# Performance work log

Hardware: AMD Instinct MI355X
Metric: run time of the kernel (lower is better)

Reference implementation:

```python
import jax, jax.numpy as jnp
import numpy as np

N, C, H, W = 64, 512, 16, 16
MEM_DIM, NUM_CLS = 2000, 10


def setup_inputs() -> dict:
    key = jax.random.key(0)
    k1, k2, k3 = jax.random.split(key, 3)
    z = jax.random.normal(k1, (N, C, H, W), dtype=jnp.float32)
    cls = jax.random.randint(k2, (N,), 0, NUM_CLS, dtype=jnp.int32)
    # nn.init.normal_(memory, 0.0, 0.02)
    memory = 0.02 * jax.random.normal(k3, (1, C, MEM_DIM, NUM_CLS), dtype=jnp.float32)
    return {"z": z, "cls": cls, "memory": memory}


def reference(z, cls, memory):
    n, c, h, w_ = z.shape
    hw = h * w_
    # memory[0,:,:,cls] -> (C, M, N) -> per-sample class memory (N, C, M)
    mem_cls = jnp.transpose(memory[0][:, :, cls], (2, 0, 1))  # (N, C, M)
    zf = z.reshape(n, c, hw)  # (N, C, HW)
    # similarity = -||z - m||^2 = 2 z.m - ||z||^2 - ||m||^2
    zm = jnp.einsum('ncp,ncm->npm', zf, mem_cls)          # (N, HW, M)
    z2 = jnp.sum(zf * zf, axis=1)[:, :, None]             # (N, HW, 1)
    m2 = jnp.sum(mem_cls * mem_cls, axis=1)[:, None, :]   # (N, 1, M)
    sim = 2.0 * zm - z2 - m2                               # (N, HW, M)
    log_w = jax.nn.log_softmax(sim, axis=2)
    w = jax.nn.softmax(sim, axis=2)
    w_hat = w  # topk == -1 in forward path
    # z_hat = bmm(mem_cls (N,C,M), w_hat^T (N,M,HW)) -> (N,C,HW)
    z_hat = jnp.einsum('ncm,npm->ncp', mem_cls, w_hat).reshape(n, c, h, w_)
    return (z_hat, w_hat, w, log_w)
```

## Files before the change

### kernel.cpp

```cpp
#include <hip/hip_runtime.h>
#include <hip/hip_bf16.h>
#include <math.h>

#define N_   64
#define C_   512
#define HW_  256
#define M_   2000
#define KCLS 10
#define MP_  2048

typedef __attribute__((ext_vector_type(8))) short bf16x8;
typedef __attribute__((ext_vector_type(4))) float f32x4;

__device__ __forceinline__ short f2bf(float x) {
    __hip_bfloat16 b = __float2bfloat16(x);
    return *reinterpret_cast<short*>(&b);
}
__device__ __forceinline__ float bf2f(short s) {
    __hip_bfloat16 b = *reinterpret_cast<__hip_bfloat16*>(&s);
    return __bfloat162float(b);
}

#define GATHER_LDS (KCLS * 32 * 66 * 2)
#define PART_LDS   (KCLS * 8 * 32 * 4)

__global__ __launch_bounds__(256) void prep_kernel(const float* __restrict__ mem,
                                                   const float* __restrict__ z,
                                                   const int* __restrict__ cls,
                                                   short* __restrict__ mcm,
                                                   short* __restrict__ mmc,
                                                   short* __restrict__ zTb,
                                                   float* __restrict__ m2,
                                                   int* __restrict__ perm) {
    __shared__ __align__(16) char smem[GATHER_LDS + PART_LDS];
    const int t = threadIdx.x;
    const int bid = blockIdx.x;

    if (bid < 512) {
        short (*tile)[32][66] = reinterpret_cast<short(*)[32][66]>(smem);
        float (*part)[8][32]  = reinterpret_cast<float(*)[8][32]>(smem + GATHER_LDS);
        const int m0 = (bid & 63) * 32;
        const int c0 = (bid >> 6) * 64;
        const int mm = t & 31;
        const int m = m0 + mm;
        const int cbase = t >> 5;
        float msum[KCLS];
#pragma unroll
        for (int k = 0; k < KCLS; ++k) msum[k] = 0.f;
        for (int ci = 0; ci < 8; ++ci) {
            const int cl = cbase + ci * 8;
            const int c = c0 + cl;
            short v[KCLS];
            if (m < M_) {
                const float* src = mem + ((size_t)c * M_ + m) * KCLS;
#pragma unroll
                for (int k = 0; k < KCLS; ++k) v[k] = f2bf(src[k]);
            } else {
#pragma unroll
                for (int k = 0; k < KCLS; ++k) v[k] = 0;
            }
#pragma unroll
            for (int k = 0; k < KCLS; ++k) {
                mcm[(size_t)k * (C_ * MP_) + (size_t)c * MP_ + m] = v[k];
                tile[k][mm][cl] = v[k];
                const float f = bf2f(v[k]);
                msum[k] = fmaf(f, f, msum[k]);
            }
        }
#pragma unroll
        for (int k = 0; k < KCLS; ++k) part[k][cbase][mm] = msum[k];
        __syncthreads();
        for (int idx = t; idx < KCLS * 32; idx += 256) {
            const int k = idx >> 5, mr = idx & 31;
            float s = 0.f;
#pragma unroll
            for (int cb = 0; cb < 8; ++cb) s += part[k][cb][mr];
            atomicAdd(&m2[k * MP_ + m0 + mr], s);
        }
        const int cc = t & 63;
        const int rbase = t >> 6;
        for (int k = 0; k < KCLS; ++k) {
#pragma unroll
            for (int r = 0; r < 8; ++r) {
                const int mm2 = r * 4 + rbase;
                mmc[(size_t)k * (MP_ * C_) + (size_t)(m0 + mm2) * C_ + c0 + cc] =
                    tile[k][mm2][cc];
            }
        }
    } else if (bid < 2560) {
        short (*tile)[70] = reinterpret_cast<short(*)[70]>(smem);
        const int b = bid - 512;
        const int c0 = (b & 7) * 64;
        const int p0 = ((b >> 3) & 3) * 64;
        const int n = b >> 5;
        const float* zp = z + (size_t)n * C_ * HW_;
        const int pp = t & 63;
        const int cb = t >> 6;
#pragma unroll
        for (int i = 0; i < 16; ++i) {
            const int cl = i * 4 + cb;
            tile[cl][pp] = f2bf(zp[(size_t)(c0 + cl) * HW_ + p0 + pp]);
        }
        __syncthreads();
        short* dst = zTb + (size_t)n * HW_ * C_;
        const int cc = t & 63;
        const int pb = t >> 6;
#pragma unroll
        for (int i = 0; i < 16; ++i) {
            const int pl = i * 4 + pb;
            dst[(size_t)(p0 + pl) * C_ + c0 + cc] = tile[cc][pl];
        }
    } else {
        int* lcls = reinterpret_cast<int*>(smem);
        if (t < N_) lcls[t] = cls[t];
        __syncthreads();
        if (t == 0) {
            int cnt[KCLS], pos[KCLS];
#pragma unroll
            for (int k = 0; k < KCLS; ++k) cnt[k] = 0;
            for (int n = 0; n < N_; ++n) cnt[lcls[n]]++;
            int acc = 0;
#pragma unroll
            for (int k = 0; k < KCLS; ++k) { pos[k] = acc; acc += cnt[k]; }
            for (int n = 0; n < N_; ++n) perm[pos[lcls[n]]++] = n;
        }
    }
}

__global__ __launch_bounds__(256) void simp_kernel(
    const short* __restrict__ zTb, const short* __restrict__ mmc,
    const int* __restrict__ cls, const int* __restrict__ perm,
    const float* __restrict__ m2, short* __restrict__ P,
    float* __restrict__ rowsum)
{
    constexpr int GX = 16, GY = 2;
    constexpr int CPX = GX * GY * N_ / 8;

    const int flat = blockIdx.x + GX * (blockIdx.y + GY * blockIdx.z);
    const int logical = (flat & 7) * CPX + (flat >> 3);
    const int nl = logical / (GX * GY);
    const int n  = perm[nl];
    const int rr = logical % (GX * GY);
    const int by = rr / GX, bx = rr % GX;

    const int kc = cls[n];
    const int rowA0 = by * 128, colB0 = bx * 128;

    const short* A = zTb + (size_t)n * HW_ * C_;
    const short* B = mmc + (size_t)kc * MP_ * C_;

    __shared__ short smem[2 * 128 * 64];
    short* As = smem;
    short* Bs = smem + 128 * 64;

    const int tid = threadIdx.x;
    const int w = tid >> 6, lane = tid & 63;
    const int wr = w >> 1, wc = w & 1;
    const int srow = lane >> 3, sslot = lane & 7;
    const int lo = lane & 15, hi = lane >> 4;

    f32x4 acc[4][4];
#pragma unroll
    for (int i = 0; i < 4; ++i)
#pragma unroll
        for (int j = 0; j < 4; ++j) acc[i][j] = (f32x4){0.f, 0.f, 0.f, 0.f};

    for (int k0 = 0; k0 < C_; k0 += 64) {
#pragma unroll
        for (int i = 0; i < 4; ++i) {
            const int row = w * 32 + i * 8 + srow;
            const int chunk = sslot ^ (row & 7);
            const short* srcA = A + (size_t)(rowA0 + row) * C_ + k0 + (chunk << 3);
            __builtin_amdgcn_global_load_lds(
                (const __attribute__((address_space(1))) void*)srcA,
                (__attribute__((address_space(3))) void*)&As[(w * 32 + i * 8) * 64],
                16, 0, 0);
            const short* srcB = B + (size_t)(colB0 + row) * C_ + k0 + (chunk << 3);
            __builtin_amdgcn_global_load_lds(
                (const __attribute__((address_space(1))) void*)srcB,
                (__attribute__((address_space(3))) void*)&Bs[(w * 32 + i * 8) * 64],
                16, 0, 0);
        }
        __syncthreads();
        bf16x8 a[4][2], b[4][2];
#pragma unroll
        for (int i = 0; i < 4; ++i)
#pragma unroll
            for (int kk = 0; kk < 2; ++kk) {
                const int ra = wr * 64 + i * 16 + lo;
                const int slot = kk * 4 + hi;
                a[i][kk] = *reinterpret_cast<const bf16x8*>(&As[ra * 64 + ((slot ^ (ra & 7)) << 3)]);
                const int rb = wc * 64 + i * 16 + lo;
                b[i][kk] = *reinterpret_cast<const bf16x8*>(&Bs[rb * 64 + ((slot ^ (rb & 7)) << 3)]);
            }
#pragma unroll
        for (int i = 0; i < 4; ++i)
#pragma unroll
            for (int j = 0; j < 4; ++j)
#pragma unroll
                for (int kk = 0; kk < 2; ++kk)
                    acc[i][j] = __builtin_amdgcn_mfma_f32_16x16x32_bf16(a[i][kk], b[j][kk], acc[i][j], 0, 0, 0);
        __syncthreads();
    }

    float rs[4][4];
#pragma unroll
    for (int i = 0; i < 4; ++i)
#pragma unroll
        for (int r = 0; r < 4; ++r) rs[i][r] = 0.f;

    short* outs = smem;
#pragma unroll
    for (int i = 0; i < 4; ++i)
#pragma unroll
        for (int j = 0; j < 4; ++j) {
            const int col = wc * 64 + j * 16 + lo;
            const int mg = colB0 + col;
            const float m2v = m2[kc * MP_ + mg];
#pragma unroll
            for (int r = 0; r < 4; ++r) {
                const int row = wr * 64 + i * 16 + hi * 4 + r;
                const float s = 2.f * acc[i][j][r] - m2v;
                const float pv = (mg < M_) ? __expf(fminf(s, 60.f)) : 0.f;
                rs[i][r] += pv;
                outs[row * 128 + (col ^ (((row >> 2) & 7) << 3))] = f2bf(pv);
            }
        }
#pragma unroll
    for (int i = 0; i < 4; ++i)
#pragma unroll
        for (int r = 0; r < 4; ++r) {
            float v = rs[i][r];
            v += __shfl_xor(v, 1); v += __shfl_xor(v, 2);
            v += __shfl_xor(v, 4); v += __shfl_xor(v, 8);
            if (lo == 0)
                atomicAdd(&rowsum[n * HW_ + rowA0 + wr * 64 + i * 16 + hi * 4 + r], v);
        }
    __syncthreads();
    short* myP = P + (size_t)(n * HW_ + rowA0) * MP_ + colB0;
#pragma unroll
    for (int it = 0; it < 8; ++it) {
        const int chunk = tid + it * 256;
        const int row = chunk >> 4, c8 = (chunk & 15) * 8;
        bf16x8 v = *reinterpret_cast<const bf16x8*>(
            &outs[row * 128 + (c8 ^ (((row >> 2) & 7) << 3))]);
        *reinterpret_cast<bf16x8*>(myP + (size_t)row * MP_ + c8) = v;
    }
}

__global__ __launch_bounds__(256) void zhat_kernel(
    const short* __restrict__ mcm, const short* __restrict__ P,
    const int* __restrict__ cls, const int* __restrict__ perm,
    const float* __restrict__ rowsum, float* __restrict__ zhat)
{
    const int flat = blockIdx.x;
    const int logical = (flat & 7) * 64 + (flat >> 3);
    const int nl = logical >> 3;
    const int rr = logical & 7;
    const int n = perm[nl];
    const int kc = cls[n];
    const int ct = rr >> 1, ptb = rr & 1;
    const int rowA0 = ct * 128, colB0 = ptb * 128;

    const short* A = mcm + (size_t)kc * C_ * MP_;
    const short* B = P + (size_t)n * HW_ * MP_;
    float* D = zhat + (size_t)n * C_ * HW_;

    __shared__ short smem[2 * 128 * 64];
    short* As = smem;
    short* Bs = smem + 128 * 64;

    const int tid = threadIdx.x;
    const int w = tid >> 6, lane = tid & 63;
    const int wr = w >> 1, wc = w & 1;
    const int srow = lane >> 3, sslot = lane & 7;

    f32x4 acc[4][4];
#pragma unroll
    for (int i = 0; i < 4; ++i)
#pragma unroll
        for (int j = 0; j < 4; ++j) acc[i][j] = (f32x4){0.f, 0.f, 0.f, 0.f};

    for (int k0 = 0; k0 < MP_; k0 += 64) {
#pragma unroll
        for (int i = 0; i < 4; ++i) {
            const int row = w * 32 + i * 8 + srow;
            const int chunk = sslot ^ (row & 7);
            const short* srcA = A + (size_t)(rowA0 + row) * MP_ + k0 + (chunk << 3);
            __builtin_amdgcn_global_load_lds(
                (const __attribute__((address_space(1))) void*)srcA,
                (__attribute__((address_space(3))) void*)&As[(w * 32 + i * 8) * 64],
                16, 0, 0);
            const short* srcB = B + (size_t)(colB0 + row) * MP_ + k0 + (chunk << 3);
            __builtin_amdgcn_global_load_lds(
                (const __attribute__((address_space(1))) void*)srcB,
                (__attribute__((address_space(3))) void*)&Bs[(w * 32 + i * 8) * 64],
                16, 0, 0);
        }
        __syncthreads();
        bf16x8 a[4][2], b[4][2];
#pragma unroll
        for (int i = 0; i < 4; ++i)
#pragma unroll
            for (int kk = 0; kk < 2; ++kk) {
                const int ra = wr * 64 + i * 16 + (lane & 15);
                const int slot = kk * 4 + (lane >> 4);
                a[i][kk] = *reinterpret_cast<const bf16x8*>(&As[ra * 64 + ((slot ^ (ra & 7)) << 3)]);
                const int rb = wc * 64 + i * 16 + (lane & 15);
                b[i][kk] = *reinterpret_cast<const bf16x8*>(&Bs[rb * 64 + ((slot ^ (rb & 7)) << 3)]);
            }
#pragma unroll
        for (int i = 0; i < 4; ++i)
#pragma unroll
            for (int j = 0; j < 4; ++j)
#pragma unroll
                for (int kk = 0; kk < 2; ++kk)
                    acc[i][j] = __builtin_amdgcn_mfma_f32_16x16x32_bf16(a[i][kk], b[j][kk], acc[i][j], 0, 0, 0);
        __syncthreads();
    }

    float alpha[4];
#pragma unroll
    for (int j = 0; j < 4; ++j)
        alpha[j] = 1.f / rowsum[n * HW_ + colB0 + wc * 64 + j * 16 + (lane & 15)];

    float* outf = (float*)smem;
#pragma unroll
    for (int h = 0; h < 2; ++h) {
        if (wr == h) {
#pragma unroll
            for (int i = 0; i < 4; ++i)
#pragma unroll
                for (int j = 0; j < 4; ++j) {
                    const int col = wc * 64 + j * 16 + (lane & 15);
#pragma unroll
                    for (int r = 0; r < 4; ++r) {
                        const int row = i * 16 + (lane >> 4) * 4 + r;
                        outf[row * 128 + (col ^ (((row >> 2) & 1) << 4))] = acc[i][j][r] * alpha[j];
                    }
                }
        }
        __syncthreads();
#pragma unroll
        for (int it = 0; it < 8; ++it) {
            const int chunk = tid + it * 256;
            const int row = chunk >> 5, c4 = (chunk & 31) * 4;
            float4 v = *reinterpret_cast<const float4*>(
                &outf[row * 128 + (c4 ^ (((row >> 2) & 1) << 4))]);
            *reinterpret_cast<float4*>(
                &D[(size_t)(rowA0 + h * 64 + row) * HW_ + colB0 + c4]) = v;
        }
        __syncthreads();
    }
}

__global__ __launch_bounds__(256) void finish_kernel(const short* __restrict__ P,
                                                     const float* __restrict__ rowsum,
                                                     float* __restrict__ w_hat,
                                                     float* __restrict__ w,
                                                     float* __restrict__ logw) {
    const int r = blockIdx.x;
    const int t = threadIdx.x;
    if (t >= (M_ / 8)) return;
    bf16x8 v = *reinterpret_cast<const bf16x8*>(P + (size_t)r * MP_ + t * 8);
    const float gsum = rowsum[r];
    const float inv = 1.f / gsum;
    const float lg = __logf(gsum);
    float pf[8];
#pragma unroll
    for (int q = 0; q < 8; ++q) pf[q] = bf2f(v[q]);
    float4 w0, w1, l0, l1;
    w0.x = pf[0] * inv; w0.y = pf[1] * inv; w0.z = pf[2] * inv; w0.w = pf[3] * inv;
    w1.x = pf[4] * inv; w1.y = pf[5] * inv; w1.z = pf[6] * inv; w1.w = pf[7] * inv;
    l0.x = __logf(pf[0]) - lg; l0.y = __logf(pf[1]) - lg;
    l0.z = __logf(pf[2]) - lg; l0.w = __logf(pf[3]) - lg;
    l1.x = __logf(pf[4]) - lg; l1.y = __logf(pf[5]) - lg;
    l1.z = __logf(pf[6]) - lg; l1.w = __logf(pf[7]) - lg;
    const size_t ob = (size_t)r * M_ + t * 8;
    *reinterpret_cast<float4*>(w + ob)         = w0;
    *reinterpret_cast<float4*>(w + ob + 4)     = w1;
    *reinterpret_cast<float4*>(w_hat + ob)     = w0;
    *reinterpret_cast<float4*>(w_hat + ob + 4) = w1;
    *reinterpret_cast<float4*>(logw + ob)      = l0;
    *reinterpret_cast<float4*>(logw + ob + 4)  = l1;
}

extern "C" void kernel_launch(void* const* d_in, const int* in_sizes, int n_in,
                              void* d_out, int out_size, void* d_ws, size_t ws_size,
                              hipStream_t stream) {
    const float* z      = (const float*)d_in[0];
    const int*   cls    = (const int*)d_in[1];
    const float* memory = (const float*)d_in[2];

    float* out   = (float*)d_out;
    float* z_hat = out;
    float* w_hat = z_hat + (size_t)N_ * C_ * HW_;
    float* w     = w_hat + (size_t)N_ * HW_ * M_;
    float* logw  = w     + (size_t)N_ * HW_ * M_;

    const size_t mcm_sh = (size_t)KCLS * C_ * MP_;
    const size_t mmc_sh = mcm_sh;
    const size_t zTb_sh = (size_t)N_ * HW_ * C_;
    const size_t P_sh   = (size_t)N_ * HW_ * MP_;
    const size_t m2_fl  = (size_t)KCLS * MP_;
    const size_t rs_fl  = (size_t)N_ * HW_;
    const size_t need_main = (mcm_sh + mmc_sh + zTb_sh + P_sh) * 2
                           + (m2_fl + rs_fl) * 4 + 256;

    short *mcm, *mmc, *zTb, *P;
    float *m2, *rowsum;
    int* perm;
    if (ws_size >= need_main) {
        char* p = (char*)d_ws;
        m2     = (float*)p;  p += m2_fl * 4;
        rowsum = (float*)p;  p += rs_fl * 4;
        perm   = (int*)p;    p += 256;
        mcm    = (short*)p;  p += mcm_sh * 2;
        mmc    = (short*)p;  p += mmc_sh * 2;
        zTb    = (short*)p;  p += zTb_sh * 2;
        P      = (short*)p;
    } else {
        char* p = (char*)d_ws;
        m2     = (float*)p;  p += m2_fl * 4;
        rowsum = (float*)p;  p += rs_fl * 4;
        perm   = (int*)p;    p += 256;
        P      = (short*)p;
        char* q = (char*)w_hat;
        mcm    = (short*)q;  q += mcm_sh * 2;
        mmc    = (short*)q;
        zTb    = (short*)z_hat;
    }

    hipMemsetAsync(m2, 0, (m2_fl + rs_fl) * sizeof(float), stream);
    prep_kernel<<<2561, 256, 0, stream>>>(memory, z, cls, mcm, mmc, zTb, m2, perm);
    simp_kernel<<<dim3(16, 2, N_), 256, 0, stream>>>(zTb, mmc, cls, perm, m2, P, rowsum);
    zhat_kernel<<<512, 256, 0, stream>>>(mcm, P, cls, perm, rowsum, z_hat);
    finish_kernel<<<N_ * HW_, 256, 0, stream>>>(P, rowsum, w_hat, w, logw);
}
```

Before: 257.2 us.

## Merge z_hat GEMM and softmax finish into one heterogeneous tail kernel

Launches a single tail kernel whose first 512 blocks run the z_hat GEMM and whose remaining 1024 blocks each normalize 16 softmax rows, writing w, w_hat and log_w. This removes a kernel boundary and lets the compute-bound GEMM overlap with the bandwidth-bound finish work. Each finish block now also handles 16 rows instead of one. All blocks reserve the GEMM's shared-memory allocation, which can lower occupancy for the finish blocks. The fallback path used when workspace is small keeps two separate launches.

Measured after the change: 276.2 us. +7.4%, slower.

```diff
diff --git a/kernel.cpp b/kernel.cpp
--- a/kernel.cpp
+++ b/kernel.cpp
@@ -248,12 +248,12 @@
     }
 }
 
-__global__ __launch_bounds__(256) void zhat_kernel(
+__device__ __forceinline__ void zhat_body(
     const short* __restrict__ mcm, const short* __restrict__ P,
     const int* __restrict__ cls, const int* __restrict__ perm,
-    const float* __restrict__ rowsum, float* __restrict__ zhat)
-{
-    const int flat = blockIdx.x;
+    const float* __restrict__ rowsum, float* __restrict__ zhat,
+    short* smem, const int flat)
+{
     const int logical = (flat & 7) * 64 + (flat >> 3);
     const int nl = logical >> 3;
     const int rr = logical & 7;
@@ -266,7 +266,6 @@
     const short* B = P + (size_t)n * HW_ * MP_;
     float* D = zhat + (size_t)n * C_ * HW_;
 
-    __shared__ short smem[2 * 128 * 64];
     short* As = smem;
     short* Bs = smem + 128 * 64;
 
@@ -354,35 +353,67 @@
     }
 }
 
-__global__ __launch_bounds__(256) void finish_kernel(const short* __restrict__ P,
-                                                     const float* __restrict__ rowsum,
-                                                     float* __restrict__ w_hat,
-                                                     float* __restrict__ w,
-                                                     float* __restrict__ logw) {
-    const int r = blockIdx.x;
+__device__ __forceinline__ void finish_rows(
+    const short* __restrict__ P, const float* __restrict__ rowsum,
+    float* __restrict__ w_hat, float* __restrict__ w,
+    float* __restrict__ logw, const int row0, const int nrows)
+{
     const int t = threadIdx.x;
     if (t >= (M_ / 8)) return;
-    bf16x8 v = *reinterpret_cast<const bf16x8*>(P + (size_t)r * MP_ + t * 8);
-    const float gsum = rowsum[r];
-    const float inv = 1.f / gsum;
-    const float lg = __logf(gsum);
-    float pf[8];
-#pragma unroll
-    for (int q = 0; q < 8; ++q) pf[q] = bf2f(v[q]);
-    float4 w0, w1, l0, l1;
-    w0.x = pf[0] * inv; w0.y = pf[1] * inv; w0.z = pf[2] * inv; w0.w = pf[3] * inv;
-    w1.x = pf[4] * inv; w1.y = pf[5] * inv; w1.z = pf[6] * inv; w1.w = pf[7] * inv;
-    l0.x = __logf(pf[0]) - lg; l0.y = __logf(pf[1]) - lg;
-    l0.z = __logf(pf[2]) - lg; l0.w = __logf(pf[3]) - lg;
-    l1.x = __logf(pf[4]) - lg; l1.y = __logf(pf[5]) - lg;
-    l1.z = __logf(pf[6]) - lg; l1.w = __logf(pf[7]) - lg;
-    const size_t ob = (size_t)r * M_ + t * 8;
-    *reinterpret_cast<float4*>(w + ob)         = w0;
-    *reinterpret_cast<float4*>(w + ob + 4)     = w1;
-    *reinterpret_cast<float4*>(w_hat + ob)     = w0;
-    *reinterpret_cast<float4*>(w_hat + ob + 4) = w1;
-    *reinterpret_cast<float4*>(logw + ob)      = l0;
-    *reinterpret_cast<float4*>(logw + ob + 4)  = l1;
+    for (int i = 0; i < nrows; ++i) {
+        const int r = row0 + i;
+        bf16x8 v = *reinterpret_cast<const bf16x8*>(P + (size_t)r * MP_ + t * 8);
+        const float gsum = rowsum[r];
+        const float inv = 1.f / gsum;
+        const float lg = __logf(gsum);
+        float pf[8];
+#pragma unroll
+        for (int q = 0; q < 8; ++q) pf[q] = bf2f(v[q]);
+        float4 w0, w1, l0, l1;
+        w0.x = pf[0] * inv; w0.y = pf[1] * inv; w0.z = pf[2] * inv; w0.w = pf[3] * inv;
+        w1.x = pf[4] * inv; w1.y = pf[5] * inv; w1.z = pf[6] * inv; w1.w = pf[7] * inv;
+        l0.x = __logf(pf[0]) - lg; l0.y = __logf(pf[1]) - lg;
+        l0.z = __logf(pf[2]) - lg; l0.w = __logf(pf[3]) - lg;
+        l1.x = __logf(pf[4]) - lg; l1.y = __logf(pf[5]) - lg;
+        l1.z = __logf(pf[6]) - lg; l1.w = __logf(pf[7]) - lg;
+        const size_t ob = (size_t)r * M_ + t * 8;
+        *reinterpret_cast<float4*>(w + ob)         = w0;
+        *reinterpret_cast<float4*>(w + ob + 4)     = w1;
+        *reinterpret_cast<float4*>(w_hat + ob)     = w0;
+        *reinterpret_cast<float4*>(w_hat + ob + 4) = w1;
+        *reinterpret_cast<float4*>(logw + ob)      = l0;
+        *reinterpret_cast<float4*>(logw + ob + 4)  = l1;
+    }
+}
+
+__global__ __launch_bounds__(256) void tail_kernel(
+    const short* __restrict__ mcm, const short* __restrict__ P,
+    const int* __restrict__ cls, const int* __restrict__ perm,
+    const float* __restrict__ rowsum, float* __restrict__ zhat,
+    float* __restrict__ w_hat, float* __restrict__ w, float* __restrict__ logw)
+{
+    __shared__ short smem[2 * 128 * 64];
+    if (blockIdx.x < 512) {
+        zhat_body(mcm, P, cls, perm, rowsum, zhat, smem, blockIdx.x);
+    } else {
+        finish_rows(P, rowsum, w_hat, w, logw, (blockIdx.x - 512) * 16, 16);
+    }
+}
+
+__global__ __launch_bounds__(256) void zhat_kernel(
+    const short* __restrict__ mcm, const short* __restrict__ P,
+    const int* __restrict__ cls, const int* __restrict__ perm,
+    const float* __restrict__ rowsum, float* __restrict__ zhat)
+{
+    __shared__ short smem[2 * 128 * 64];
+    zhat_body(mcm, P, cls, perm, rowsum, zhat, smem, blockIdx.x);
+}
+
+__global__ __launch_bounds__(256) void finish_kernel(
+    const short* __restrict__ P, const float* __restrict__ rowsum,
+    float* __restrict__ w_hat, float* __restrict__ w, float* __restrict__ logw)
+{
+    finish_rows(P, rowsum, w_hat, w, logw, blockIdx.x * 16, 16);
 }
 
 extern "C" void kernel_launch(void* const* d_in, const int* in_sizes, int n_in,
@@ -410,6 +441,7 @@
     short *mcm, *mmc, *zTb, *P;
     float *m2, *rowsum;
     int* perm;
+    int merged;
     if (ws_size >= need_main) {
         char* p = (char*)d_ws;
         m2     = (float*)p;  p += m2_fl * 4;
@@ -419,6 +451,7 @@
         mmc    = (short*)p;  p += mmc_sh * 2;
         zTb    = (short*)p;  p += zTb_sh * 2;
         P      = (short*)p;
+        merged = 1;
     } else {
         char* p = (char*)d_ws;
         m2     = (float*)p;  p += m2_fl * 4;
@@ -429,11 +462,17 @@
         mcm    = (short*)q;  q += mcm_sh * 2;
         mmc    = (short*)q;
         zTb    = (short*)z_hat;
+        merged = 0;
     }
 
     hipMemsetAsync(m2, 0, (m2_fl + rs_fl) * sizeof(float), stream);
     prep_kernel<<<2561, 256, 0, stream>>>(memory, z, cls, mcm, mmc, zTb, m2, perm);
     simp_kernel<<<dim3(16, 2, N_), 256, 0, stream>>>(zTb, mmc, cls, perm, m2, P, rowsum);
-    zhat_kernel<<<512, 256, 0, stream>>>(mcm, P, cls, perm, rowsum, z_hat);
-    finish_kernel<<<N_ * HW_, 256, 0, stream>>>(P, rowsum, w_hat, w, logw);
-}
+    if (merged) {
+        tail_kernel<<<1536, 256, 0, stream>>>(mcm, P, cls, perm, rowsum,
+                                              z_hat, w_hat, w, logw);
+    } else {
+        zhat_kernel<<<512, 256, 0, stream>>>(mcm, P, cls, perm, rowsum, z_hat);
+        finish_kernel<<<N_ * HW_ / 16, 256, 0, stream>>>(P, rowsum, w_hat, w, logw);
+    }
+}
```

## Replace atomic reductions with partial-sum buffers and drop memset launch

Applied to the files above, without the earlier changes.

Column norms (m2) and softmax row sums are now written as per-block partial arrays, 8 channel groups and 16 column tiles respectively, instead of being accumulated with atomicAdd into a zeroed buffer. Consumers sum the partials on read. This removes the hipMemsetAsync launch and the atomic traffic. The finish kernel also processes 16 rows per block, cutting the grid size. The cost is more redundant global reads of partials in simp, zhat and finish, plus a larger workspace.

Result: slower. 273.5 us (+6.3%).

```diff
diff --git a/kernel.cpp b/kernel.cpp
--- a/kernel.cpp
+++ b/kernel.cpp
@@ -8,6 +8,7 @@
 #define M_   2000
 #define KCLS 10
 #define MP_  2048
+#define NHW  (N_ * HW_)
 
 typedef __attribute__((ext_vector_type(8))) short bf16x8;
 typedef __attribute__((ext_vector_type(4))) float f32x4;
@@ -30,7 +31,7 @@
                                                    short* __restrict__ mcm,
                                                    short* __restrict__ mmc,
                                                    short* __restrict__ zTb,
-                                                   float* __restrict__ m2,
+                                                   float* __restrict__ m2p,
                                                    int* __restrict__ perm) {
     __shared__ __align__(16) char smem[GATHER_LDS + PART_LDS];
     const int t = threadIdx.x;
@@ -41,6 +42,7 @@
         float (*part)[8][32]  = reinterpret_cast<float(*)[8][32]>(smem + GATHER_LDS);
         const int m0 = (bid & 63) * 32;
         const int c0 = (bid >> 6) * 64;
+        const int cg = bid >> 6;
         const int mm = t & 31;
         const int m = m0 + mm;
         const int cbase = t >> 5;
@@ -75,7 +77,7 @@
             float s = 0.f;
 #pragma unroll
             for (int cb = 0; cb < 8; ++cb) s += part[k][cb][mr];
-            atomicAdd(&m2[k * MP_ + m0 + mr], s);
+            m2p[(size_t)(cg * KCLS + k) * MP_ + m0 + mr] = s;
         }
         const int cc = t & 63;
         const int rbase = t >> 6;
@@ -130,8 +132,8 @@
 __global__ __launch_bounds__(256) void simp_kernel(
     const short* __restrict__ zTb, const short* __restrict__ mmc,
     const int* __restrict__ cls, const int* __restrict__ perm,
-    const float* __restrict__ m2, short* __restrict__ P,
-    float* __restrict__ rowsum)
+    const float* __restrict__ m2p, short* __restrict__ P,
+    float* __restrict__ rspart)
 {
     constexpr int GX = 16, GY = 2;
     constexpr int CPX = GX * GY * N_ / 8;
@@ -150,6 +152,7 @@
     const short* B = mmc + (size_t)kc * MP_ * C_;
 
     __shared__ short smem[2 * 128 * 64];
+    __shared__ float rsL[128][2];
     short* As = smem;
     short* Bs = smem + 128 * 64;
 
@@ -216,7 +219,10 @@
         for (int j = 0; j < 4; ++j) {
             const int col = wc * 64 + j * 16 + lo;
             const int mg = colB0 + col;
-            const float m2v = m2[kc * MP_ + mg];
+            float m2v = 0.f;
+#pragma unroll
+            for (int cg = 0; cg < 8; ++cg)
+                m2v += m2p[(size_t)(cg * KCLS + kc) * MP_ + mg];
 #pragma unroll
             for (int r = 0; r < 4; ++r) {
                 const int row = wr * 64 + i * 16 + hi * 4 + r;
@@ -233,10 +239,11 @@
             float v = rs[i][r];
             v += __shfl_xor(v, 1); v += __shfl_xor(v, 2);
             v += __shfl_xor(v, 4); v += __shfl_xor(v, 8);
-            if (lo == 0)
-                atomicAdd(&rowsum[n * HW_ + rowA0 + wr * 64 + i * 16 + hi * 4 + r], v);
+            if (lo == 0) rsL[wr * 64 + i * 16 + hi * 4 + r][wc] = v;
         }
     __syncthreads();
+    if (tid < 128)
+        rspart[(size_t)bx * NHW + n * HW_ + rowA0 + tid] = rsL[tid][0] + rsL[tid][1];
     short* myP = P + (size_t)(n * HW_ + rowA0) * MP_ + colB0;
 #pragma unroll
     for (int it = 0; it < 8; ++it) {
@@ -251,7 +258,7 @@
 __global__ __launch_bounds__(256) void zhat_kernel(
     const short* __restrict__ mcm, const short* __restrict__ P,
     const int* __restrict__ cls, const int* __restrict__ perm,
-    const float* __restrict__ rowsum, float* __restrict__ zhat)
+    const float* __restrict__ rspart, float* __restrict__ zhat)
 {
     const int flat = blockIdx.x;
     const int logical = (flat & 7) * 64 + (flat >> 3);
@@ -321,8 +328,13 @@
 
     float alpha[4];
 #pragma unroll
-    for (int j = 0; j < 4; ++j)
-        alpha[j] = 1.f / rowsum[n * HW_ + colB0 + wc * 64 + j * 16 + (lane & 15)];
+    for (int j = 0; j < 4; ++j) {
+        const int rrow = n * HW_ + colB0 + wc * 64 + j * 16 + (lane & 15);
+        float s = 0.f;
+#pragma unroll
+        for (int q = 0; q < 16; ++q) s += rspart[(size_t)q * NHW + rrow];
+        alpha[j] = 1.f / s;
+    }
 
     float* outf = (float*)smem;
 #pragma unroll
@@ -354,35 +366,39 @@
     }
 }
 
-__global__ __launch_bounds__(256) void finish_kernel(const short* __restrict__ P,
-                                                     const float* __restrict__ rowsum,
-                                                     float* __restrict__ w_hat,
-                                                     float* __restrict__ w,
-                                                     float* __restrict__ logw) {
-    const int r = blockIdx.x;
+__global__ __launch_bounds__(256) void finish_kernel(
+    const short* __restrict__ P, const float* __restrict__ rspart,
+    float* __restrict__ w_hat, float* __restrict__ w, float* __restrict__ logw)
+{
     const int t = threadIdx.x;
     if (t >= (M_ / 8)) return;
-    bf16x8 v = *reinterpret_cast<const bf16x8*>(P + (size_t)r * MP_ + t * 8);
-    const float gsum = rowsum[r];
-    const float inv = 1.f / gsum;
-    const float lg = __logf(gsum);
-    float pf[8];
-#pragma unroll
-    for (int q = 0; q < 8; ++q) pf[q] = bf2f(v[q]);
-    float4 w0, w1, l0, l1;
-    w0.x = pf[0] * inv; w0.y = pf[1] * inv; w0.z = pf[2] * inv; w0.w = pf[3] * inv;
-    w1.x = pf[4] * inv; w1.y = pf[5] * inv; w1.z = pf[6] * inv; w1.w = pf[7] * inv;
-    l0.x = __logf(pf[0]) - lg; l0.y = __logf(pf[1]) - lg;
-    l0.z = __logf(pf[2]) - lg; l0.w = __logf(pf[3]) - lg;
-    l1.x = __logf(pf[4]) - lg; l1.y = __logf(pf[5]) - lg;
-    l1.z = __logf(pf[6]) - lg; l1.w = __logf(pf[7]) - lg;
-    const size_t ob = (size_t)r * M_ + t * 8;
-    *reinterpret_cast<float4*>(w + ob)         = w0;
-    *reinterpret_cast<float4*>(w + ob + 4)     = w1;
-    *reinterpret_cast<float4*>(w_hat + ob)     = w0;
-    *reinterpret_cast<float4*>(w_hat + ob + 4) = w1;
-    *reinterpret_cast<float4*>(logw + ob)      = l0;
-    *reinterpret_cast<float4*>(logw + ob + 4)  = l1;
+    const int row0 = blockIdx.x * 16;
+    for (int i = 0; i < 16; ++i) {
+        const int r = row0 + i;
+        bf16x8 v = *reinterpret_cast<const bf16x8*>(P + (size_t)r * MP_ + t * 8);
+        float gsum = 0.f;
+#pragma unroll
+        for (int q = 0; q < 16; ++q) gsum += rspart[(size_t)q * NHW + r];
+        const float inv = 1.f / gsum;
+        const float lg = __logf(gsum);
+        float pf[8];
+#pragma unroll
+        for (int q = 0; q < 8; ++q) pf[q] = bf2f(v[q]);
+        float4 w0, w1, l0, l1;
+        w0.x = pf[0] * inv; w0.y = pf[1] * inv; w0.z = pf[2] * inv; w0.w = pf[3] * inv;
+        w1.x = pf[4] * inv; w1.y = pf[5] * inv; w1.z = pf[6] * inv; w1.w = pf[7] * inv;
+        l0.x = __logf(pf[0]) - lg; l0.y = __logf(pf[1]) - lg;
+        l0.z = __logf(pf[2]) - lg; l0.w = __logf(pf[3]) - lg;
+        l1.x = __logf(pf[4]) - lg; l1.y = __logf(pf[5]) - lg;
+        l1.z = __logf(pf[6]) - lg; l1.w = __logf(pf[7]) - lg;
+        const size_t ob = (size_t)r * M_ + t * 8;
+        *reinterpret_cast<float4*>(w + ob)         = w0;
+        *reinterpret_cast<float4*>(w + ob + 4)     = w1;
+        *reinterpret_cast<float4*>(w_hat + ob)     = w0;
+        *reinterpret_cast<float4*>(w_hat + ob + 4) = w1;
+        *reinterpret_cast<float4*>(logw + ob)      = l0;
+        *reinterpret_cast<float4*>(logw + ob + 4)  = l1;
+    }
 }
 
 extern "C" void kernel_launch(void* const* d_in, const int* in_sizes, int n_in,
@@ -402,18 +418,18 @@
     const size_t mmc_sh = mcm_sh;
     const size_t zTb_sh = (size_t)N_ * HW_ * C_;
     const size_t P_sh   = (size_t)N_ * HW_ * MP_;
-    const size_t m2_fl  = (size_t)KCLS * MP_;
-    const size_t rs_fl  = (size_t)N_ * HW_;
+    const size_t m2p_fl = (size_t)8 * KCLS * MP_;
+    const size_t rsp_fl = (size_t)16 * NHW;
     const size_t need_main = (mcm_sh + mmc_sh + zTb_sh + P_sh) * 2
-                           + (m2_fl + rs_fl) * 4 + 256;
+                           + (m2p_fl + rsp_fl) * 4 + 256;
 
     short *mcm, *mmc, *zTb, *P;
-    float *m2, *rowsum;
+    float *m2p, *rspart;
     int* perm;
     if (ws_size >= need_main) {
         char* p = (char*)d_ws;
-        m2     = (float*)p;  p += m2_fl * 4;
-        rowsum = (float*)p;  p += rs_fl * 4;
+        m2p    = (float*)p;  p += m2p_fl * 4;
+        rspart = (float*)p;  p += rsp_fl * 4;
         perm   = (int*)p;    p += 256;
         mcm    = (short*)p;  p += mcm_sh * 2;
         mmc    = (short*)p;  p += mmc_sh * 2;
@@ -421,8 +437,8 @@
         P      = (short*)p;
     } else {
         char* p = (char*)d_ws;
-        m2     = (float*)p;  p += m2_fl * 4;
-        rowsum = (float*)p;  p += rs_fl * 4;
+        m2p    = (float*)p;  p += m2p_fl * 4;
+        rspart = (float*)p;  p += rsp_fl * 4;
         perm   = (int*)p;    p += 256;
         P      = (short*)p;
         char* q = (char*)w_hat;
@@ -431,9 +447,8 @@
         zTb    = (short*)z_hat;
     }
 
-    hipMemsetAsync(m2, 0, (m2_fl + rs_fl) * sizeof(float), stream);
-    prep_kernel<<<2561, 256, 0, stream>>>(memory, z, cls, mcm, mmc, zTb, m2, perm);
-    simp_kernel<<<dim3(16, 2, N_), 256, 0, stream>>>(zTb, mmc, cls, perm, m2, P, rowsum);
-    zhat_kernel<<<512, 256, 0, stream>>>(mcm, P, cls, perm, rowsum, z_hat);
-    finish_kernel<<<N_ * HW_, 256, 0, stream>>>(P, rowsum, w_hat, w, logw);
-}
+    prep_kernel<<<2561, 256, 0, stream>>>(memory, z, cls, mcm, mmc, zTb, m2p, perm);
+    simp_kernel<<<dim3(16, 2, N_), 256, 0, stream>>>(zTb, mmc, cls, perm, m2p, P, rspart);
+    zhat_kernel<<<512, 256, 0, stream>>>(mcm, P, cls, perm, rspart, z_hat);
+    finish_kernel<<<NHW / 16, 256, 0, stream>>>(P, rspart, w_hat, w, logw);
+}
```
